# Kernel optimization log

Measured on AMD Instinct MI355X. Metric: run time of the kernel, lower is better.

The kernel has to match this reference:

```python
import jax, jax.numpy as jnp
import numpy as np

K = 8  # in-edges per non-source node (forward direction)

def _mp_forward(y, src_local, pre_w, pre_b, upd_w, upd_b):
    # y: [L, P, D] node features by topological level; src_local: [L-1, P*K]
    L, P, D = y.shape
    # level 0 has no in-edges: builtin mean gives z = 0 -> y += relu(update(0)) = relu(b)
    y0 = jax.nn.relu(upd_b) + y[0]
    def step(y_prev, inp):
        src, y_init = inp
        msg = jax.nn.relu(y_prev[src] @ pre_w + pre_b)      # [P*K, D] gather + msg FNN
        z = msg.reshape(P, K, D).mean(axis=1)               # fn.mean reduce
        y_new = jax.nn.relu(z @ upd_w + upd_b) + y_init     # update + residual
        return y_new, y_new
    _, ys = jax.lax.scan(step, y0, (src_local, y[1:]))
    return jnp.concatenate([y0[None], ys], axis=0)

def _mp_reverse(y, src_local, pre_w, pre_b, upd_w, upd_b):
    # propagate along reversed edges, reverse topological order
    L, P, D = y.shape
    dst_local = jnp.repeat(jnp.arange(P), K)                # local dst of each fwd edge
    y_last = jax.nn.relu(upd_b) + y[-1]                     # sinks: z = 0
    def step(y_next, inp):
        src, y_init = inp
        msg = jax.nn.relu(y_next[dst_local] @ pre_w + pre_b)            # [P*K, D]
        z_sum = jax.ops.segment_sum(msg, src, num_segments=P)
        deg = jax.ops.segment_sum(jnp.ones((P * K,), msg.dtype), src, num_segments=P)
        z = z_sum / jnp.maximum(deg, 1.0)[:, None]          # mean; zero-deg -> 0
        y_new = jax.nn.relu(z @ upd_w + upd_b) + y_init
        return y_new, y_new
    _, ys = jax.lax.scan(step, y_last, (src_local, y[:-1]), reverse=True)
    return jnp.concatenate([ys, y_last[None]], axis=0)

def setup_inputs() -> dict:
    key = jax.random.key(0)
    ks = jax.random.split(key, 16)
    N, node_dim, D = 131072, 128, 128   # D = out_dim // 2
    L, P = 16, 8192
    s = 0.06
    return {
        "x": jax.random.normal(ks[0], (N, node_dim), jnp.float32),
        "src_local": jax.random.randint(ks[1], (L - 1, P * K), 0, P).astype(jnp.int32),
        "nt_w1": jax.random.normal(ks[2], (node_dim, node_dim), jnp.float32) * s,
        "nt_b1": jax.random.normal(ks[3], (node_dim,), jnp.float32) * s,
        "nt_w2": jax.random.normal(ks[4], (node_dim, D), jnp.float32) * s,
        "nt_b2": jax.random.normal(ks[5], (D,), jnp.float32) * s,
        "f_pre_w": jax.random.normal(ks[6], (D, D), jnp.float32) * s,
        "f_pre_b": jax.random.normal(ks[7], (D,), jnp.float32) * s,
        "f_upd_w": jax.random.normal(ks[8], (D, D), jnp.float32) * s,
        "f_upd_b": jax.random.normal(ks[9], (D,), jnp.float32) * s,
        "b_pre_w": jax.random.normal(ks[10], (D, D), jnp.float32) * s,
        "b_pre_b": jax.random.normal(ks[11], (D,), jnp.float32) * s,
        "b_upd_w": jax.random.normal(ks[12], (D, D), jnp.float32) * s,
        "b_upd_b": jax.random.normal(ks[13], (D,), jnp.float32) * s,
    }

def reference(x, src_local, nt_w1, nt_b1, nt_w2, nt_b2,
              f_pre_w, f_pre_b, f_upd_w, f_upd_b,
              b_pre_w, b_pre_b, b_upd_w, b_upd_b):
    Lm1, PK = src_local.shape
    P, L = PK // K, Lm1 + 1
    N = x.shape[0]
    # node_transform: FNN(node_dim, [node_dim], out_dim//2)
    h = jax.nn.relu(x @ nt_w1 + nt_b1) @ nt_w2 + nt_b2      # [N, D]
    y = h.reshape(L, P, -1)
    hf = _mp_forward(y, src_local, f_pre_w, f_pre_b, f_upd_w, f_upd_b).reshape(N, -1)
    hb = _mp_reverse(y, src_local, b_pre_w, b_pre_b, b_upd_w, b_upd_b).reshape(N, -1)
    return jnp.concatenate([hf, hb], axis=1)
```

## Files before the change

### kernel.cpp

```cpp
#include <hip/hip_runtime.h>
#include <cstddef>
#include <cstdint>

#define DD   128
#define PP   8192
#define KK   8
#define LLV  16
#define NN   131072
#define NE   65536
#define NLVL 15

typedef _Float16 h8 __attribute__((ext_vector_type(8)));
typedef _Float16 h4 __attribute__((ext_vector_type(4)));
typedef float f4v __attribute__((ext_vector_type(4)));

__device__ __forceinline__ float4 ld4(const float* p) { return *(const float4*)p; }
__device__ __forceinline__ void st4(float* p, float4 v) { *(float4*)p = v; }

__device__ __forceinline__ int swz(int row, int k) { return row * 128 + (k ^ ((row & 7) << 3)); }
__device__ __forceinline__ int uswz(int row, int c) { return row * 128 + (c ^ ((row & 7) << 2)); }

__device__ __forceinline__ void hstore4(_Float16* ah, int row, int k0, float4 v) {
  int o = swz(row, k0);
  h4 hi;
  hi[0] = (_Float16)v.x; hi[1] = (_Float16)v.y;
  hi[2] = (_Float16)v.z; hi[3] = (_Float16)v.w;
  *(h4*)(ah + o) = hi;
}

__device__ __forceinline__ void load_bfrags1(const _Float16* __restrict__ img, int t16, int lane,
                                             h8 Bh[4], h8 Bl[4]) {
#pragma unroll
  for (int ks = 0; ks < 4; ks++) {
    int o = ((t16 * 4 + ks) * 64 + lane) * 8;
    Bh[ks] = *(const h8*)(img + o);
    Bl[ks] = *(const h8*)(img + 16384 + o);
  }
}

__device__ __forceinline__ f4v gemm_rt(const _Float16* __restrict__ ah,
                                       const h8 Bh[4], const h8 Bl[4], int rbase, int lane) {
  int r16 = lane & 15, kb = lane >> 4;
  int arow = rbase + r16;
  h8 Ah[4];
#pragma unroll
  for (int ks = 0; ks < 4; ks++) Ah[ks] = *(const h8*)(ah + swz(arow, ks * 32 + kb * 8));
  f4v a = {0.f, 0.f, 0.f, 0.f};
#pragma unroll
  for (int ks = 0; ks < 4; ks++) a = __builtin_amdgcn_mfma_f32_16x16x32_f16(Ah[ks], Bh[ks], a, 0, 0, 0);
#pragma unroll
  for (int ks = 0; ks < 4; ks++) a = __builtin_amdgcn_mfma_f32_16x16x32_f16(Ah[ks], Bl[ks], a, 0, 0, 0);
  return a;
}

__global__ __launch_bounds__(1024) void setup_kernel(
    const float* __restrict__ w0, const float* __restrict__ w1,
    const float* __restrict__ w2, const float* __restrict__ w3,
    const float* __restrict__ w4, const float* __restrict__ w5,
    _Float16* __restrict__ img_base,
    const int* __restrict__ src_all,
    int* __restrict__ offs, int* __restrict__ edges) {
  int t = threadIdx.x;
  if (blockIdx.x < 12) {
    int mat = blockIdx.x >> 1;
    int g = (blockIdx.x & 1) * 1024 + t;
    const float* w;
    switch (mat) {
      case 0: w = w0; break;
      case 1: w = w1; break;
      case 2: w = w2; break;
      case 3: w = w3; break;
      case 4: w = w4; break;
      default: w = w5; break;
    }
    _Float16* img = img_base + (size_t)mat * 32768;
    int t16 = g >> 8, ks = (g >> 6) & 3, lane = g & 63;
    int n = t16 * 16 + (lane & 15);
    int kb = ks * 32 + (lane >> 4) * 8;
    h8 hi, lo;
#pragma unroll
    for (int j = 0; j < 8; j++) {
      float v = w[(kb + j) * 128 + n];
      _Float16 h = (_Float16)v;
      hi[j] = h;
      lo[j] = (_Float16)(v - (float)h);
    }
    int o = ((t16 * 4 + ks) * 64 + lane) * 8;
    *(h8*)(img + o) = hi;
    *(h8*)(img + 16384 + o) = lo;
  } else {
    int l = blockIdx.x - 12;
    const int* src = src_all + (size_t)l * NE;
    __shared__ int cnt[PP];
    __shared__ int bsum[1024];
#pragma unroll
    for (int j = 0; j < 8; j++) cnt[t + j * 1024] = 0;
    __syncthreads();
#pragma unroll 4
    for (int j = 0; j < 64; j++) {
      int q = src[j * 1024 + t];
      atomicAdd(&cnt[q], 1);
    }
    __syncthreads();
    int loc[8];
    int s = 0;
#pragma unroll
    for (int j = 0; j < 8; j++) { loc[j] = cnt[t * 8 + j]; s += loc[j]; }
    bsum[t] = s;
    __syncthreads();
    for (int off = 1; off < 1024; off <<= 1) {
      int v = (t >= off) ? bsum[t - off] : 0;
      __syncthreads();
      bsum[t] += v;
      __syncthreads();
    }
    int run = (t == 0) ? 0 : bsum[t - 1];
#pragma unroll
    for (int j = 0; j < 8; j++) {
      offs[l * (PP + 1) + t * 8 + j] = run;
      cnt[t * 8 + j] = run;
      run += loc[j];
    }
    if (t == 1023) offs[l * (PP + 1) + PP] = run;
    __syncthreads();
#pragma unroll 4
    for (int j = 0; j < 64; j++) {
      int e = j * 1024 + t;
      int q = src[e];
      int pos = atomicAdd(&cnt[q], 1);
      edges[(size_t)l * NE + pos] = e >> 3;
    }
  }
}

__global__ __launch_bounds__(512, 4) void nt_kernel(
    const float* __restrict__ x,
    const _Float16* __restrict__ w1img, const float* __restrict__ b1,
    const _Float16* __restrict__ w2img, const float* __restrict__ b2,
    float* __restrict__ hout) {
  __shared__ __align__(16) _Float16 abuf[8192];
  __shared__ __align__(16) float dbuf[8192];
  int tid = threadIdx.x;
  int lane = tid & 63, wv = tid >> 6;
  int c4 = tid & 31, rg4 = (tid >> 5) * 4;
  size_t base = (size_t)blockIdx.x * 64;

  h8 Bh[4], Bl[4];
  load_bfrags1(w1img, wv, lane, Bh, Bl);

#pragma unroll
  for (int j = 0; j < 4; j++) {
    int s = tid + j * 512;
    float4 v = ((const float4*)(x + base * 128))[s];
    hstore4(abuf, s >> 5, (s & 31) * 4, v);
  }
  __syncthreads();

  f4v acc[4];
#pragma unroll
  for (int rt = 0; rt < 4; rt++) acc[rt] = gemm_rt(abuf, Bh, Bl, rt * 16, lane);
  {
    int r16 = lane & 15, kb = lane >> 4;
    int col = wv * 16 + r16;
    float b = b1[col];
#pragma unroll
    for (int rt = 0; rt < 4; rt++)
#pragma unroll
      for (int r = 0; r < 4; r++)
        dbuf[uswz(rt * 16 + kb * 4 + r, col)] = fmaxf(acc[rt][r] + b, 0.f);
  }
  load_bfrags1(w2img, wv, lane, Bh, Bl);
  __syncthreads();

  float4 uu[4];
#pragma unroll
  for (int i = 0; i < 4; i++) uu[i] = *(const float4*)(dbuf + uswz(rg4 + i, c4 * 4));
#pragma unroll
  for (int i = 0; i < 4; i++) hstore4(abuf, rg4 + i, c4 * 4, uu[i]);
  __syncthreads();

#pragma unroll
  for (int rt = 0; rt < 4; rt++) acc[rt] = gemm_rt(abuf, Bh, Bl, rt * 16, lane);
  {
    int r16 = lane & 15, kb = lane >> 4;
    int col = wv * 16 + r16;
    float b = b2[col];
#pragma unroll
    for (int rt = 0; rt < 4; rt++)
#pragma unroll
      for (int r = 0; r < 4; r++)
        dbuf[uswz(rt * 16 + kb * 4 + r, col)] = acc[rt][r] + b;
  }
  __syncthreads();
#pragma unroll
  for (int i = 0; i < 4; i++)
    st4(hout + (base + rg4 + i) * 128 + c4 * 4, *(const float4*)(dbuf + uswz(rg4 + i, c4 * 4)));
}

__global__ __launch_bounds__(512, 4) void mp_step(
    const float* __restrict__ h,
    const int* __restrict__ src_all,
    const int* __restrict__ offs,
    const int* __restrict__ edges,
    const _Float16* __restrict__ fw_upd_img, const float* __restrict__ fw_upd_b,
    const _Float16* __restrict__ fw_pre_img, const float* __restrict__ fw_pre_b,
    const _Float16* __restrict__ bw_upd_img, const float* __restrict__ bw_upd_b,
    const _Float16* __restrict__ bw_pre_img, const float* __restrict__ bw_pre_b,
    const _Float16* __restrict__ mf_in, _Float16* __restrict__ mf_out,
    const _Float16* __restrict__ mb_in, _Float16* __restrict__ mb_out,
    float* __restrict__ out, int step) {
  __shared__ __align__(16) _Float16 abuf[4096];
  __shared__ __align__(16) float dbuf[4096];
  int tid = threadIdx.x;
  int lane = tid & 63, wv = tid >> 6;
  int c4 = tid & 31, rg2 = (tid >> 5) * 2;
  bool is_fwd = blockIdx.x < 256;
  int tile = (blockIdx.x & 255) * 32;
  int level = is_fwd ? step : 15 - step;
  const _Float16* upd_img = is_fwd ? fw_upd_img : bw_upd_img;
  const float* upd_b = is_fwd ? fw_upd_b : bw_upd_b;
  const _Float16* pre_img = is_fwd ? fw_pre_img : bw_pre_img;
  const float* pre_b = is_fwd ? fw_pre_b : bw_pre_b;
  const _Float16* m_in = is_fwd ? mf_in : mb_in;
  _Float16* m_out      = is_fwd ? mf_out : mb_out;
  bool has_mout = (step < 15);
  int col_off = is_fwd ? 0 : 128;

  float4 res[2];
#pragma unroll
  for (int i = 0; i < 2; i++) {
    int n = level * PP + tile + rg2 + i;
    res[i] = ld4(h + (size_t)n * 128 + c4 * 4);
  }

  float4 u[2];
  if (step == 0) {
    float4 bv = ld4(upd_b + c4 * 4);
    float4 rb;
    rb.x = fmaxf(bv.x, 0.f); rb.y = fmaxf(bv.y, 0.f);
    rb.z = fmaxf(bv.z, 0.f); rb.w = fmaxf(bv.w, 0.f);
#pragma unroll
    for (int i = 0; i < 2; i++) {
      u[i].x = rb.x + res[i].x; u[i].y = rb.y + res[i].y;
      u[i].z = rb.z + res[i].z; u[i].w = rb.w + res[i].w;
    }
  } else {
    h8 BhU[4], BlU[4];
    load_bfrags1(upd_img, wv, lane, BhU, BlU);

    if (is_fwd) {
      const int* src = src_all + (step - 1) * NE;
#pragma unroll
      for (int i = 0; i < 2; i++) {
        int r = rg2 + i;
        int p = tile + r;
        h4 v[8];
#pragma unroll
        for (int k = 0; k < 8; k++) {
          int sidx = src[p * 8 + k];
          v[k] = *(const h4*)(m_in + (size_t)sidx * 128 + c4 * 4);
        }
        float4 a;
        a.x = (((float)v[0][0] + (float)v[1][0]) + ((float)v[2][0] + (float)v[3][0])) +
              (((float)v[4][0] + (float)v[5][0]) + ((float)v[6][0] + (float)v[7][0]));
        a.y = (((float)v[0][1] + (float)v[1][1]) + ((float)v[2][1] + (float)v[3][1])) +
              (((float)v[4][1] + (float)v[5][1]) + ((float)v[6][1] + (float)v[7][1]));
        a.z = (((float)v[0][2] + (float)v[1][2]) + ((float)v[2][2] + (float)v[3][2])) +
              (((float)v[4][2] + (float)v[5][2]) + ((float)v[6][2] + (float)v[7][2]));
        a.w = (((float)v[0][3] + (float)v[1][3]) + ((float)v[2][3] + (float)v[3][3])) +
              (((float)v[4][3] + (float)v[5][3]) + ((float)v[6][3] + (float)v[7][3]));
        a.x *= 0.125f; a.y *= 0.125f; a.z *= 0.125f; a.w *= 0.125f;
        hstore4(abuf, r, c4 * 4, a);
      }
    } else {
      const int* off_l = offs + level * (PP + 1);
      const int* ep = edges + level * NE;
#pragma unroll
      for (int i = 0; i < 2; i++) {
        int r = rg2 + i;
        int q = tile + r;
        int e0 = off_l[q], e1 = off_l[q + 1];
        float4 a = {0.f, 0.f, 0.f, 0.f};
        int idx = e0;
        for (; idx + 4 <= e1; idx += 4) {
          int p0 = ep[idx], p1 = ep[idx + 1], p2 = ep[idx + 2], p3 = ep[idx + 3];
          h4 v0 = *(const h4*)(m_in + (size_t)p0 * 128 + c4 * 4);
          h4 v1 = *(const h4*)(m_in + (size_t)p1 * 128 + c4 * 4);
          h4 v2 = *(const h4*)(m_in + (size_t)p2 * 128 + c4 * 4);
          h4 v3 = *(const h4*)(m_in + (size_t)p3 * 128 + c4 * 4);
          a.x += ((float)v0[0] + (float)v1[0]) + ((float)v2[0] + (float)v3[0]);
          a.y += ((float)v0[1] + (float)v1[1]) + ((float)v2[1] + (float)v3[1]);
          a.z += ((float)v0[2] + (float)v1[2]) + ((float)v2[2] + (float)v3[2]);
          a.w += ((float)v0[3] + (float)v1[3]) + ((float)v2[3] + (float)v3[3]);
        }
        for (; idx < e1; idx++) {
          int p = ep[idx];
          h4 v = *(const h4*)(m_in + (size_t)p * 128 + c4 * 4);
          a.x += (float)v[0]; a.y += (float)v[1]; a.z += (float)v[2]; a.w += (float)v[3];
        }
        float inv = (e1 > e0) ? 1.0f / (float)(e1 - e0) : 0.f;
        a.x *= inv; a.y *= inv; a.z *= inv; a.w *= inv;
        hstore4(abuf, r, c4 * 4, a);
      }
    }
    __syncthreads();

    f4v acc[2];
#pragma unroll
    for (int rt = 0; rt < 2; rt++) acc[rt] = gemm_rt(abuf, BhU, BlU, rt * 16, lane);
    {
      int r16 = lane & 15, kb = lane >> 4;
      int col = wv * 16 + r16;
      float b = upd_b[col];
#pragma unroll
      for (int rt = 0; rt < 2; rt++)
#pragma unroll
        for (int r = 0; r < 4; r++)
          dbuf[uswz(rt * 16 + kb * 4 + r, col)] = fmaxf(acc[rt][r] + b, 0.f);
    }
    __syncthreads();

#pragma unroll
    for (int i = 0; i < 2; i++) {
      int r = rg2 + i;
      float4 uv = *(const float4*)(dbuf + uswz(r, c4 * 4));
      u[i].x = uv.x + res[i].x;
      u[i].y = uv.y + res[i].y;
      u[i].z = uv.z + res[i].z;
      u[i].w = uv.w + res[i].w;
    }
  }

#pragma unroll
  for (int i = 0; i < 2; i++) {
    int n = level * PP + tile + rg2 + i;
    st4(out + (size_t)n * 256 + col_off + c4 * 4, u[i]);
  }

  if (has_mout) {
    h8 BhP[4], BlP[4];
    load_bfrags1(pre_img, wv, lane, BhP, BlP);
#pragma unroll
    for (int i = 0; i < 2; i++) hstore4(abuf, rg2 + i, c4 * 4, u[i]);
    __syncthreads();
    f4v acc[2];
#pragma unroll
    for (int rt = 0; rt < 2; rt++) acc[rt] = gemm_rt(abuf, BhP, BlP, rt * 16, lane);
    {
      int r16 = lane & 15, kb = lane >> 4;
      int col = wv * 16 + r16;
      float b = pre_b[col];
#pragma unroll
      for (int rt = 0; rt < 2; rt++)
#pragma unroll
        for (int r = 0; r < 4; r++)
          dbuf[uswz(rt * 16 + kb * 4 + r, col)] = fmaxf(acc[rt][r] + b, 0.f);
    }
    __syncthreads();
#pragma unroll
    for (int i = 0; i < 2; i++) {
      int r = rg2 + i;
      float4 m = *(const float4*)(dbuf + uswz(r, c4 * 4));
      h4 mh;
      mh[0] = (_Float16)m.x; mh[1] = (_Float16)m.y;
      mh[2] = (_Float16)m.z; mh[3] = (_Float16)m.w;
      *(h4*)(m_out + (size_t)(tile + r) * 128 + c4 * 4) = mh;
    }
  }
}

extern "C" void kernel_launch(void* const* d_in, const int* in_sizes, int n_in,
                              void* d_out, int out_size, void* d_ws, size_t ws_size,
                              hipStream_t stream) {
  const float* x      = (const float*)d_in[0];
  const int*   src    = (const int*)d_in[1];
  const float* nt_w1  = (const float*)d_in[2];
  const float* nt_b1  = (const float*)d_in[3];
  const float* nt_w2  = (const float*)d_in[4];
  const float* nt_b2  = (const float*)d_in[5];
  const float* f_pre_w = (const float*)d_in[6];
  const float* f_pre_b = (const float*)d_in[7];
  const float* f_upd_w = (const float*)d_in[8];
  const float* f_upd_b = (const float*)d_in[9];
  const float* b_pre_w = (const float*)d_in[10];
  const float* b_pre_b = (const float*)d_in[11];
  const float* b_upd_w = (const float*)d_in[12];
  const float* b_upd_b = (const float*)d_in[13];
  float* out = (float*)d_out;

  float* wsf = (float*)d_ws;
  float* h   = wsf;
  _Float16* mf0 = (_Float16*)(h + (size_t)NN * DD);
  _Float16* mf1 = mf0 + (size_t)PP * DD;
  _Float16* mb0 = mf1 + (size_t)PP * DD;
  _Float16* mb1 = mb0 + (size_t)PP * DD;
  int* offs   = (int*)(mb1 + (size_t)PP * DD);
  int* edges  = offs + NLVL * (PP + 1);

  uintptr_t ip = (uintptr_t)(edges + (size_t)NLVL * NE);
  ip = (ip + 15) & ~(uintptr_t)15;
  _Float16* img = (_Float16*)ip;
  _Float16* i_ntw1 = img;
  _Float16* i_ntw2 = img + 32768;
  _Float16* i_fupd = img + 2 * 32768;
  _Float16* i_fpre = img + 3 * 32768;
  _Float16* i_bupd = img + 4 * 32768;
  _Float16* i_bpre = img + 5 * 32768;

  setup_kernel<<<27, 1024, 0, stream>>>(nt_w1, nt_w2, f_upd_w, f_pre_w, b_upd_w, b_pre_w,
                                        img, src, offs, edges);
  nt_kernel<<<NN / 64, 512, 0, stream>>>(x, i_ntw1, nt_b1, i_ntw2, nt_b2, h);

  for (int s = 0; s < 16; s++) {
    const _Float16* mf_in = (s & 1) ? mf0 : mf1;
    _Float16* mf_out      = (s & 1) ? mf1 : mf0;
    const _Float16* mb_in = (s & 1) ? mb0 : mb1;
    _Float16* mb_out      = (s & 1) ? mb1 : mb0;
    mp_step<<<512, 512, 0, stream>>>(h, src, offs, edges,
                                     i_fupd, f_upd_b, i_fpre, f_pre_b,
                                     i_bupd, b_upd_b, i_bpre, b_pre_b,
                                     mf_in, mf_out, mb_in, mb_out, out, s);
  }
}
```

Measured before the change: 536.5 us.

## Fuse level-0/15 step into node transform and drop smem staging in mp_step

Step 0 of both directions (bias-only update plus pre-message GEMM) moves into the node-transform kernel for the first and last level blocks, which removes one mp_step launch. mp_step now writes its output and the fp16 message directly from MFMA accumulator layout and reads the residual h per element, so the fp32 staging buffer and one barrier go away. A second half-precision LDS buffer holds the update output for the pre GEMM. The trade-off is scattered, less coalesced global stores and h reads, and extra work in a subset of nt_kernel blocks.

```diff
diff --git a/kernel.cpp b/kernel.cpp
--- a/kernel.cpp
+++ b/kernel.cpp
@@ -137,7 +137,13 @@
     const float* __restrict__ x,
     const _Float16* __restrict__ w1img, const float* __restrict__ b1,
     const _Float16* __restrict__ w2img, const float* __restrict__ b2,
-    float* __restrict__ hout) {
+    float* __restrict__ hout,
+    const float* __restrict__ f_upd_b, const _Float16* __restrict__ f_pre_img,
+    const float* __restrict__ f_pre_b,
+    const float* __restrict__ b_upd_b, const _Float16* __restrict__ b_pre_img,
+    const float* __restrict__ b_pre_b,
+    _Float16* __restrict__ mf0, _Float16* __restrict__ mb0,
+    float* __restrict__ out) {
   __shared__ __align__(16) _Float16 abuf[8192];
   __shared__ __align__(16) float dbuf[8192];
   int tid = threadIdx.x;
@@ -195,6 +201,49 @@
 #pragma unroll
   for (int i = 0; i < 4; i++)
     st4(hout + (base + rg4 + i) * 128 + c4 * 4, *(const float4*)(dbuf + uswz(rg4 + i, c4 * 4)));
+
+  bool lvl0 = (blockIdx.x < 128);
+  bool lvl15 = (blockIdx.x >= 1920);
+  if (lvl0 || lvl15) {
+    const float* ub = lvl0 ? f_upd_b : b_upd_b;
+    const _Float16* pimg = lvl0 ? f_pre_img : b_pre_img;
+    const float* pb = lvl0 ? f_pre_b : b_pre_b;
+    _Float16* mdst = lvl0 ? mf0 : mb0;
+    int coloff = lvl0 ? 0 : 128;
+    size_t lbase = lvl0 ? 0 : (size_t)15 * PP;
+
+    float4 bv = ld4(ub + c4 * 4);
+    float4 rb;
+    rb.x = fmaxf(bv.x, 0.f); rb.y = fmaxf(bv.y, 0.f);
+    rb.z = fmaxf(bv.z, 0.f); rb.w = fmaxf(bv.w, 0.f);
+    float4 u[4];
+#pragma unroll
+    for (int i = 0; i < 4; i++) {
+      int row = rg4 + i;
+      float4 hv = *(const float4*)(dbuf + uswz(row, c4 * 4));
+      u[i].x = hv.x + rb.x; u[i].y = hv.y + rb.y;
+      u[i].z = hv.z + rb.z; u[i].w = hv.w + rb.w;
+      st4(out + (base + row) * 256 + coloff + c4 * 4, u[i]);
+      hstore4(abuf, row, c4 * 4, u[i]);
+    }
+    load_bfrags1(pimg, wv, lane, Bh, Bl);
+    __syncthreads();
+#pragma unroll
+    for (int rt = 0; rt < 4; rt++) acc[rt] = gemm_rt(abuf, Bh, Bl, rt * 16, lane);
+    {
+      int r16 = lane & 15, kb = lane >> 4;
+      int col = wv * 16 + r16;
+      float b = pb[col];
+#pragma unroll
+      for (int rt = 0; rt < 4; rt++)
+#pragma unroll
+        for (int r = 0; r < 4; r++) {
+          int row = rt * 16 + kb * 4 + r;
+          float m = fmaxf(acc[rt][r] + b, 0.f);
+          mdst[(base + row - lbase) * 128 + col] = (_Float16)m;
+        }
+    }
+  }
 }
 
 __global__ __launch_bounds__(512, 4) void mp_step(
@@ -209,11 +258,13 @@
     const _Float16* __restrict__ mf_in, _Float16* __restrict__ mf_out,
     const _Float16* __restrict__ mb_in, _Float16* __restrict__ mb_out,
     float* __restrict__ out, int step) {
-  __shared__ __align__(16) _Float16 abuf[4096];
-  __shared__ __align__(16) float dbuf[4096];
+  __shared__ __align__(16) _Float16 abuf0[4096];
+  __shared__ __align__(16) _Float16 abuf1[4096];
   int tid = threadIdx.x;
   int lane = tid & 63, wv = tid >> 6;
   int c4 = tid & 31, rg2 = (tid >> 5) * 2;
+  int r16 = lane & 15, kb = lane >> 4;
+  int colg = wv * 16 + r16;
   bool is_fwd = blockIdx.x < 256;
   int tile = (blockIdx.x & 255) * 32;
   int level = is_fwd ? step : 15 - step;
@@ -226,146 +277,103 @@
   bool has_mout = (step < 15);
   int col_off = is_fwd ? 0 : 128;
 
-  float4 res[2];
-#pragma unroll
-  for (int i = 0; i < 2; i++) {
-    int n = level * PP + tile + rg2 + i;
-    res[i] = ld4(h + (size_t)n * 128 + c4 * 4);
-  }
-
-  float4 u[2];
-  if (step == 0) {
-    float4 bv = ld4(upd_b + c4 * 4);
-    float4 rb;
-    rb.x = fmaxf(bv.x, 0.f); rb.y = fmaxf(bv.y, 0.f);
-    rb.z = fmaxf(bv.z, 0.f); rb.w = fmaxf(bv.w, 0.f);
-#pragma unroll
-    for (int i = 0; i < 2; i++) {
-      u[i].x = rb.x + res[i].x; u[i].y = rb.y + res[i].y;
-      u[i].z = rb.z + res[i].z; u[i].w = rb.w + res[i].w;
-    }
-  } else {
-    h8 BhU[4], BlU[4];
-    load_bfrags1(upd_img, wv, lane, BhU, BlU);
-
-    if (is_fwd) {
-      const int* src = src_all + (step - 1) * NE;
-#pragma unroll
-      for (int i = 0; i < 2; i++) {
-        int r = rg2 + i;
-        int p = tile + r;
-        h4 v[8];
-#pragma unroll
-        for (int k = 0; k < 8; k++) {
-          int sidx = src[p * 8 + k];
-          v[k] = *(const h4*)(m_in + (size_t)sidx * 128 + c4 * 4);
-        }
-        float4 a;
-        a.x = (((float)v[0][0] + (float)v[1][0]) + ((float)v[2][0] + (float)v[3][0])) +
-              (((float)v[4][0] + (float)v[5][0]) + ((float)v[6][0] + (float)v[7][0]));
-        a.y = (((float)v[0][1] + (float)v[1][1]) + ((float)v[2][1] + (float)v[3][1])) +
-              (((float)v[4][1] + (float)v[5][1]) + ((float)v[6][1] + (float)v[7][1]));
-        a.z = (((float)v[0][2] + (float)v[1][2]) + ((float)v[2][2] + (float)v[3][2])) +
-              (((float)v[4][2] + (float)v[5][2]) + ((float)v[6][2] + (float)v[7][2]));
-        a.w = (((float)v[0][3] + (float)v[1][3]) + ((float)v[2][3] + (float)v[3][3])) +
-              (((float)v[4][3] + (float)v[5][3]) + ((float)v[6][3] + (float)v[7][3]));
-        a.x *= 0.125f; a.y *= 0.125f; a.z *= 0.125f; a.w *= 0.125f;
-        hstore4(abuf, r, c4 * 4, a);
-      }
-    } else {
-      const int* off_l = offs + level * (PP + 1);
-      const int* ep = edges + level * NE;
-#pragma unroll
-      for (int i = 0; i < 2; i++) {
-        int r = rg2 + i;
-        int q = tile + r;
-        int e0 = off_l[q], e1 = off_l[q + 1];
-        float4 a = {0.f, 0.f, 0.f, 0.f};
-        int idx = e0;
-        for (; idx + 4 <= e1; idx += 4) {
-          int p0 = ep[idx], p1 = ep[idx + 1], p2 = ep[idx + 2], p3 = ep[idx + 3];
-          h4 v0 = *(const h4*)(m_in + (size_t)p0 * 128 + c4 * 4);
-          h4 v1 = *(const h4*)(m_in + (size_t)p1 * 128 + c4 * 4);
-          h4 v2 = *(const h4*)(m_in + (size_t)p2 * 128 + c4 * 4);
-          h4 v3 = *(const h4*)(m_in + (size_t)p3 * 128 + c4 * 4);
-          a.x += ((float)v0[0] + (float)v1[0]) + ((float)v2[0] + (float)v3[0]);
-          a.y += ((float)v0[1] + (float)v1[1]) + ((float)v2[1] + (float)v3[1]);
-          a.z += ((float)v0[2] + (float)v1[2]) + ((float)v2[2] + (float)v3[2]);
-          a.w += ((float)v0[3] + (float)v1[3]) + ((float)v2[3] + (float)v3[3]);
-        }
-        for (; idx < e1; idx++) {
-          int p = ep[idx];
-          h4 v = *(const h4*)(m_in + (size_t)p * 128 + c4 * 4);
-          a.x += (float)v[0]; a.y += (float)v[1]; a.z += (float)v[2]; a.w += (float)v[3];
-        }
-        float inv = (e1 > e0) ? 1.0f / (float)(e1 - e0) : 0.f;
-        a.x *= inv; a.y *= inv; a.z *= inv; a.w *= inv;
-        hstore4(abuf, r, c4 * 4, a);
-      }
-    }
-    __syncthreads();
-
-    f4v acc[2];
-#pragma unroll
-    for (int rt = 0; rt < 2; rt++) acc[rt] = gemm_rt(abuf, BhU, BlU, rt * 16, lane);
-    {
-      int r16 = lane & 15, kb = lane >> 4;
-      int col = wv * 16 + r16;
-      float b = upd_b[col];
-#pragma unroll
-      for (int rt = 0; rt < 2; rt++)
-#pragma unroll
-        for (int r = 0; r < 4; r++)
-          dbuf[uswz(rt * 16 + kb * 4 + r, col)] = fmaxf(acc[rt][r] + b, 0.f);
-    }
-    __syncthreads();
-
+  h8 BhU[4], BlU[4];
+  load_bfrags1(upd_img, wv, lane, BhU, BlU);
+
+  if (is_fwd) {
+    const int* src = src_all + (size_t)(step - 1) * NE;
 #pragma unroll
     for (int i = 0; i < 2; i++) {
       int r = rg2 + i;
-      float4 uv = *(const float4*)(dbuf + uswz(r, c4 * 4));
-      u[i].x = uv.x + res[i].x;
-      u[i].y = uv.y + res[i].y;
-      u[i].z = uv.z + res[i].z;
-      u[i].w = uv.w + res[i].w;
-    }
-  }
-
-#pragma unroll
-  for (int i = 0; i < 2; i++) {
-    int n = level * PP + tile + rg2 + i;
-    st4(out + (size_t)n * 256 + col_off + c4 * 4, u[i]);
+      int p = tile + r;
+      const int4* sp = (const int4*)(src + p * 8);
+      int4 s0 = sp[0], s1 = sp[1];
+      h4 v0 = *(const h4*)(m_in + (size_t)s0.x * 128 + c4 * 4);
+      h4 v1 = *(const h4*)(m_in + (size_t)s0.y * 128 + c4 * 4);
+      h4 v2 = *(const h4*)(m_in + (size_t)s0.z * 128 + c4 * 4);
+      h4 v3 = *(const h4*)(m_in + (size_t)s0.w * 128 + c4 * 4);
+      h4 v4 = *(const h4*)(m_in + (size_t)s1.x * 128 + c4 * 4);
+      h4 v5 = *(const h4*)(m_in + (size_t)s1.y * 128 + c4 * 4);
+      h4 v6 = *(const h4*)(m_in + (size_t)s1.z * 128 + c4 * 4);
+      h4 v7 = *(const h4*)(m_in + (size_t)s1.w * 128 + c4 * 4);
+      float4 a;
+      a.x = (((float)v0[0] + (float)v1[0]) + ((float)v2[0] + (float)v3[0])) +
+            (((float)v4[0] + (float)v5[0]) + ((float)v6[0] + (float)v7[0]));
+      a.y = (((float)v0[1] + (float)v1[1]) + ((float)v2[1] + (float)v3[1])) +
+            (((float)v4[1] + (float)v5[1]) + ((float)v6[1] + (float)v7[1]));
+      a.z = (((float)v0[2] + (float)v1[2]) + ((float)v2[2] + (float)v3[2])) +
+            (((float)v4[2] + (float)v5[2]) + ((float)v6[2] + (float)v7[2]));
+      a.w = (((float)v0[3] + (float)v1[3]) + ((float)v2[3] + (float)v3[3])) +
+            (((float)v4[3] + (float)v5[3]) + ((float)v6[3] + (float)v7[3]));
+      a.x *= 0.125f; a.y *= 0.125f; a.z *= 0.125f; a.w *= 0.125f;
+      hstore4(abuf0, r, c4 * 4, a);
+    }
+  } else {
+    const int* off_l = offs + level * (PP + 1);
+    const int* ep = edges + level * NE;
+#pragma unroll
+    for (int i = 0; i < 2; i++) {
+      int r = rg2 + i;
+      int q = tile + r;
+      int e0 = off_l[q], e1 = off_l[q + 1];
+      float4 a = {0.f, 0.f, 0.f, 0.f};
+      int idx = e0;
+      for (; idx + 4 <= e1; idx += 4) {
+        int p0 = ep[idx], p1 = ep[idx + 1], p2 = ep[idx + 2], p3 = ep[idx + 3];
+        h4 v0 = *(const h4*)(m_in + (size_t)p0 * 128 + c4 * 4);
+        h4 v1 = *(const h4*)(m_in + (size_t)p1 * 128 + c4 * 4);
+        h4 v2 = *(const h4*)(m_in + (size_t)p2 * 128 + c4 * 4);
+        h4 v3 = *(const h4*)(m_in + (size_t)p3 * 128 + c4 * 4);
+        a.x += ((float)v0[0] + (float)v1[0]) + ((float)v2[0] + (float)v3[0]);
+        a.y += ((float)v0[1] + (float)v1[1]) + ((float)v2[1] + (float)v3[1]);
+        a.z += ((float)v0[2] + (float)v1[2]) + ((float)v2[2] + (float)v3[2]);
+        a.w += ((float)v0[3] + (float)v1[3]) + ((float)v2[3] + (float)v3[3]);
+      }
+      for (; idx < e1; idx++) {
+        int p = ep[idx];
+        h4 v = *(const h4*)(m_in + (size_t)p * 128 + c4 * 4);
+        a.x += (float)v[0]; a.y += (float)v[1]; a.z += (float)v[2]; a.w += (float)v[3];
+      }
+      float inv = (e1 > e0) ? 1.0f / (float)(e1 - e0) : 0.f;
+      a.x *= inv; a.y *= inv; a.z *= inv; a.w *= inv;
+      hstore4(abuf0, r, c4 * 4, a);
+    }
+  }
+  __syncthreads();
+
+  f4v acc[2];
+#pragma unroll
+  for (int rt = 0; rt < 2; rt++) acc[rt] = gemm_rt(abuf0, BhU, BlU, rt * 16, lane);
+  {
+    float ubs = upd_b[colg];
+#pragma unroll
+    for (int rt = 0; rt < 2; rt++)
+#pragma unroll
+      for (int r = 0; r < 4; r++) {
+        int row = rt * 16 + kb * 4 + r;
+        size_t n = (size_t)level * PP + tile + row;
+        float hv = h[n * 128 + colg];
+        float uval = fmaxf(acc[rt][r] + ubs, 0.f) + hv;
+        out[n * 256 + col_off + colg] = uval;
+        abuf1[swz(row, colg)] = (_Float16)uval;
+      }
   }
 
   if (has_mout) {
     h8 BhP[4], BlP[4];
     load_bfrags1(pre_img, wv, lane, BhP, BlP);
-#pragma unroll
-    for (int i = 0; i < 2; i++) hstore4(abuf, rg2 + i, c4 * 4, u[i]);
-    __syncthreads();
-    f4v acc[2];
-#pragma unroll
-    for (int rt = 0; rt < 2; rt++) acc[rt] = gemm_rt(abuf, BhP, BlP, rt * 16, lane);
-    {
-      int r16 = lane & 15, kb = lane >> 4;
-      int col = wv * 16 + r16;
-      float b = pre_b[col];
-#pragma unroll
-      for (int rt = 0; rt < 2; rt++)
-#pragma unroll
-        for (int r = 0; r < 4; r++)
-          dbuf[uswz(rt * 16 + kb * 4 + r, col)] = fmaxf(acc[rt][r] + b, 0.f);
-    }
-    __syncthreads();
-#pragma unroll
-    for (int i = 0; i < 2; i++) {
-      int r = rg2 + i;
-      float4 m = *(const float4*)(dbuf + uswz(r, c4 * 4));
-      h4 mh;
-      mh[0] = (_Float16)m.x; mh[1] = (_Float16)m.y;
-      mh[2] = (_Float16)m.z; mh[3] = (_Float16)m.w;
-      *(h4*)(m_out + (size_t)(tile + r) * 128 + c4 * 4) = mh;
-    }
+    __syncthreads();
+#pragma unroll
+    for (int rt = 0; rt < 2; rt++) acc[rt] = gemm_rt(abuf1, BhP, BlP, rt * 16, lane);
+    float pbs = pre_b[colg];
+#pragma unroll
+    for (int rt = 0; rt < 2; rt++)
+#pragma unroll
+      for (int r = 0; r < 4; r++) {
+        int row = rt * 16 + kb * 4 + r;
+        float m = fmaxf(acc[rt][r] + pbs, 0.f);
+        m_out[(size_t)(tile + row) * 128 + colg] = (_Float16)m;
+      }
   }
 }
 
@@ -409,9 +417,12 @@
 
   setup_kernel<<<27, 1024, 0, stream>>>(nt_w1, nt_w2, f_upd_w, f_pre_w, b_upd_w, b_pre_w,
                                         img, src, offs, edges);
-  nt_kernel<<<NN / 64, 512, 0, stream>>>(x, i_ntw1, nt_b1, i_ntw2, nt_b2, h);
-
-  for (int s = 0; s < 16; s++) {
+  nt_kernel<<<NN / 64, 512, 0, stream>>>(x, i_ntw1, nt_b1, i_ntw2, nt_b2, h,
+                                         f_upd_b, i_fpre, f_pre_b,
+                                         b_upd_b, i_bpre, b_pre_b,
+                                         mf0, mb0, out);
+
+  for (int s = 1; s < 16; s++) {
     const _Float16* mf_in = (s & 1) ? mf0 : mf1;
     _Float16* mf_out      = (s & 1) ? mf1 : mf0;
     const _Float16* mb_in = (s & 1) ? mb0 : mb1;
```

Result: faster. 523.2 us, median of 2 (-2.5%).
